# Kernel tuning notes

Measured on AMD Instinct MI355X. Metric: run time of the kernel, lower is better.

Reference implementation:

```python
import jax, jax.numpy as jnp
import numpy as np

N_NODES = 100000


def gcn_layer(x, edge_index, W, b):
    # GCNConv: out = D^{-1/2} (A + I) D^{-1/2} (x W) + b
    N = x.shape[0]
    loop = jnp.arange(N, dtype=edge_index.dtype)
    src = jnp.concatenate([edge_index[0], loop])
    dst = jnp.concatenate([edge_index[1], loop])
    deg = jax.ops.segment_sum(jnp.ones_like(src, dtype=x.dtype), dst, num_segments=N)
    dinv = jnp.where(deg > 0, jax.lax.rsqrt(deg), 0.0)
    norm = dinv[src] * dinv[dst]  # [E+N]
    h = x @ W  # [N, out]
    msg = h[src] * norm[:, None]  # [E+N, out]
    out = jax.ops.segment_sum(msg, dst, num_segments=N)
    return out + b


def setup_inputs() -> dict:
    key = jax.random.key(0)
    ks = jax.random.split(key, 8)
    x = jax.random.normal(ks[0], (N_NODES, 128), dtype=jnp.float32)
    edge_index = jax.random.randint(ks[1], (2, 1600000), 0, N_NODES, dtype=jnp.int32)
    def glorot(k, fan_in, fan_out):
        s = jnp.sqrt(6.0 / (fan_in + fan_out)).astype(jnp.float32)
        return jax.random.uniform(k, (fan_in, fan_out), jnp.float32, -s, s)
    return {
        "x": x,
        "edge_index": edge_index,
        "W1": glorot(ks[2], 128, 64), "b1": jnp.zeros((64,), jnp.float32),
        "W2": glorot(ks[3], 64, 128), "b2": jnp.zeros((128,), jnp.float32),
        "W3": glorot(ks[4], 128, 64), "b3": jnp.zeros((64,), jnp.float32),
    }


def reference(x, edge_index, W1, b1, W2, b2, W3, b3):
    h = jax.nn.relu(gcn_layer(x, edge_index, W1, b1))
    h = jax.nn.relu(gcn_layer(h, edge_index, W2, b2))
    out = gcn_layer(h, edge_index, W3, b3)
    return out
```

## Files before the change

kernel.cpp:

```cpp
#include <hip/hip_runtime.h>
#include <hip/hip_fp16.h>
#include <stdint.h>


#define NWGA 256
#define CMAX 8

typedef _Float16 half8 __attribute__((ext_vector_type(8)));
typedef float f32x4 __attribute__((ext_vector_type(4)));

struct __align__(8) Half4 { __half x, y, z, w; };

__global__ __launch_bounds__(256) void bucket_hist_kernel(
    const int* __restrict__ dst, int E, int chunk, int NBUK,
    int* __restrict__ M ) {
  __shared__ int hist[512];
  const int w = blockIdx.x, t = threadIdx.x;
  for (int i = t; i < NBUK; i += 256) hist[i] = 0;
  __syncthreads();
  const int e0 = w * chunk;
  const int e1 = min(e0 + chunk, E);
  for (int e = e0 + t; e < e1; e += 256) atomicAdd(&hist[dst[e] >> 8], 1);
  __syncthreads();
  for (int i = t; i < NBUK; i += 256) M[i * NWGA + w] = hist[i];
}

__global__ void scan_blocksum(const int* __restrict__ data, int len,
                              int* __restrict__ bsum) {
  __shared__ int s[256];
  int i = blockIdx.x * 256 + threadIdx.x;
  s[threadIdx.x] = (i < len) ? data[i] : 0;
  __syncthreads();
  for (int off = 128; off > 0; off >>= 1) {
    if (threadIdx.x < off) s[threadIdx.x] += s[threadIdx.x + off];
    __syncthreads();
  }
  if (threadIdx.x == 0) bsum[blockIdx.x] = s[0];
}

__global__ void scan_bsums(int* bsum, int NB) {
  __shared__ int s[512];
  int t = threadIdx.x;
  int v = (t < NB) ? bsum[t] : 0;
  s[t] = v;
  __syncthreads();
  for (int off = 1; off < 512; off <<= 1) {
    int u = (t >= off) ? s[t - off] : 0;
    __syncthreads();
    s[t] += u;
    __syncthreads();
  }
  if (t < NB) bsum[t] = s[t] - v;
}

__global__ void scan_final(int* __restrict__ data, int len,
                           const int* __restrict__ bsum) {
  __shared__ int s[256];
  int t = threadIdx.x;
  int i = blockIdx.x * 256 + t;
  int v = (i < len) ? data[i] : 0;
  s[t] = v;
  __syncthreads();
  for (int off = 1; off < 256; off <<= 1) {
    int u = (t >= off) ? s[t - off] : 0;
    __syncthreads();
    s[t] += u;
    __syncthreads();
  }
  if (i < len) data[i] = bsum[blockIdx.x] + s[t] - v;
}

__global__ __launch_bounds__(256) void bucket_scatter_kernel(
    const int* __restrict__ ei, int E, int chunk, int NBUK,
    const int* __restrict__ Mscan, int2* __restrict__ edata1) {
  __shared__ int cur[512];
  const int w = blockIdx.x, t = threadIdx.x;
  for (int i = t; i < NBUK; i += 256) cur[i] = Mscan[i * NWGA + w];
  __syncthreads();
  const int e0 = w * chunk;
  const int e1 = min(e0 + chunk, E);
  for (int e = e0 + t; e < e1; e += 256) {
    int s = ei[e];
    int d = ei[E + e];
    int pos = atomicAdd(&cur[d >> 8], 1);
    edata1[pos] = make_int2(s, d);
  }
}

__global__ __launch_bounds__(256) void bucket_deg_kernel(
    const int2* __restrict__ edata1, const int* __restrict__ Mscan, int E,
    int N, int NBUK, int* __restrict__ deg_arr, float* __restrict__ dinv,
    int* __restrict__ bsum2) {
  __shared__ int hist[256];
  __shared__ int red[256];
  const int b = blockIdx.x, t = threadIdx.x;
  const int ebase = Mscan[b * NWGA];
  const int eend = (b + 1 < NBUK) ? Mscan[(b + 1) * NWGA] : E;
  const int nodebase = b << 8;
  const int node = nodebase + t;
  hist[t] = 0;
  __syncthreads();
  for (int e = ebase + t; e < eend; e += 256)
    atomicAdd(&hist[edata1[e].y - nodebase], 1);
  __syncthreads();
  int pd = 0;
  if (node < N) {
    int dt = hist[t] + 1;
    pd = dt + (dt & 1);
    deg_arr[node] = dt;
    dinv[node] = rsqrtf((float)dt);
  }
  red[t] = pd;
  __syncthreads();
  for (int off = 128; off > 0; off >>= 1) {
    if (t < off) red[t] += red[t + off];
    __syncthreads();
  }
  if (t == 0) bsum2[b] = red[0];
}

__global__ void bucket_base_scan(int* bsum2, int NBUK, int* offsets, int N) {
  __shared__ int s[512];
  int t = threadIdx.x;
  int v = (t < NBUK) ? bsum2[t] : 0;
  s[t] = v;
  __syncthreads();
  for (int off = 1; off < 512; off <<= 1) {
    int u = (t >= off) ? s[t - off] : 0;
    __syncthreads();
    s[t] += u;
    __syncthreads();
  }
  if (t < NBUK) bsum2[t] = s[t] - v;
  if (t == NBUK - 1) offsets[N] = s[t];
}

__global__ __launch_bounds__(256) void bucket_fill_kernel(
    const int2* __restrict__ edata1, const int* __restrict__ Mscan,
    const int* __restrict__ deg_arr, const int* __restrict__ bsum2, int E,
    int N, int NBUK, int* __restrict__ offsets, int* __restrict__ ed3) {
  __shared__ int scan[256];
  __shared__ int cursor[256];
  const int b = blockIdx.x, t = threadIdx.x;
  const int ebase = Mscan[b * NWGA];
  const int eend = (b + 1 < NBUK) ? Mscan[(b + 1) * NWGA] : E;
  const int nodebase = b << 8;
  const int node = nodebase + t;
  const int dt = (node < N) ? deg_arr[node] : 0;
  const int pd = dt + (dt & 1);
  scan[t] = pd;
  __syncthreads();
  for (int off = 1; off < 256; off <<= 1) {
    int u = (t >= off) ? scan[t - off] : 0;
    __syncthreads();
    scan[t] += u;
    __syncthreads();
  }
  const int base = bsum2[b] + scan[t] - pd;
  cursor[t] = base + 1;
  if (node < N) {
    offsets[node] = base;
    ed3[base] = node << 7;
    if (dt & 1) ed3[base + dt] = N << 7;
  }
  __syncthreads();
  for (int e = ebase + t; e < eend; e += 256) {
    int2 sd = edata1[e];
    int pos = atomicAdd(&cursor[sd.y - nodebase], 1);
    ed3[pos] = sd.x << 7;
  }
}

__global__ void zero_rows_kernel(_Float16* a, _Float16* b) {
  if (threadIdx.x < 64) a[threadIdx.x] = (_Float16)0.f;
  else b[threadIdx.x - 64] = (_Float16)0.f;
}

template <int K, int D, bool BR, bool DSCALE, typename InT>
__global__ __launch_bounds__(256) void gemm_mfma(
    const InT* __restrict__ X, const float* __restrict__ W,
    const float* __restrict__ bias, const float* __restrict__ dinv,
    _Float16* __restrict__ H, int N) {
  __shared__ char lds[2 * K * D];
  const int t = threadIdx.x;
  for (int idx = t; idx < K * D; idx += 256) {
    const int k = idx % K;
    const int d = idx / K;
    const _Float16 v = (_Float16)W[k * D + d];
    const int byte =
        d * (2 * K) + ((((k >> 3) ^ (d & 7)) << 4) | ((k & 7) << 1));
    *(_Float16*)(lds + byte) = v;
  }
  __syncthreads();

  const int w = t >> 6;
  const int l = t & 63;
  const int lrow = l & 15;
  const int lg = l >> 4;
  const int r0 = blockIdx.x * 128 + w * 32;
  if (r0 >= N) return;

  f32x4 acc[2][D / 16];
#pragma unroll
  for (int rt = 0; rt < 2; ++rt)
#pragma unroll
    for (int c = 0; c < D / 16; ++c) acc[rt][c] = (f32x4){0.f, 0.f, 0.f, 0.f};

  int rA[2];
  rA[0] = min(r0 + lrow, N - 1);
  rA[1] = min(r0 + 16 + lrow, N - 1);

#pragma unroll
  for (int s = 0; s < K / 32; ++s) {
    half8 a[2];
#pragma unroll
    for (int rt = 0; rt < 2; ++rt) {
      if constexpr (sizeof(InT) == 2) {
        a[rt] = *reinterpret_cast<const half8*>(
            (const _Float16*)X + (size_t)rA[rt] * K + s * 32 + lg * 8);
      } else {
        const float* xp = (const float*)X + (size_t)rA[rt] * K + s * 32 + lg * 8;
        float4 lo = *reinterpret_cast<const float4*>(xp);
        float4 hi = *reinterpret_cast<const float4*>(xp + 4);
        half8 af;
        af[0] = (_Float16)lo.x; af[1] = (_Float16)lo.y;
        af[2] = (_Float16)lo.z; af[3] = (_Float16)lo.w;
        af[4] = (_Float16)hi.x; af[5] = (_Float16)hi.y;
        af[6] = (_Float16)hi.z; af[7] = (_Float16)hi.w;
        a[rt] = af;
      }
    }
    half8 b[D / 16];
#pragma unroll
    for (int c = 0; c < D / 16; ++c) {
      const int d = c * 16 + lrow;
      const int g = s * 4 + lg;
      b[c] = *reinterpret_cast<const half8*>(
          lds + d * (2 * K) + (((g ^ (d & 7)) << 4)));
    }
#pragma unroll
    for (int rt = 0; rt < 2; ++rt)
#pragma unroll
      for (int c = 0; c < D / 16; ++c)
        acc[rt][c] = __builtin_amdgcn_mfma_f32_16x16x32_f16(a[rt], b[c],
                                                            acc[rt][c], 0, 0, 0);
  }

  float bv[D / 16];
  if (BR) {
#pragma unroll
    for (int c = 0; c < D / 16; ++c) bv[c] = bias[c * 16 + lrow];
  }
#pragma unroll
  for (int rt = 0; rt < 2; ++rt) {
#pragma unroll
    for (int r = 0; r < 4; ++r) {
      const int row = r0 + rt * 16 + lg * 4 + r;
      if (row < N) {
        float ds = 1.f;
        if (DSCALE) ds = dinv[row];
#pragma unroll
        for (int c = 0; c < D / 16; ++c) {
          float v = acc[rt][c][r];
          if (BR) v = fmaxf(v + bv[c], 0.f);
          if (DSCALE) v *= ds;
          H[(size_t)row * D + c * 16 + lrow] = (_Float16)v;
        }
      }
    }
  }
}

template <bool BIAS, bool RELU, bool SCALE_OUT, typename OutT>
__global__ __launch_bounds__(256) void agg_kernel(
    const __half* __restrict__ h, const int* __restrict__ ed,
    const int* __restrict__ offsets, const float* __restrict__ dinv,
    const float* __restrict__ bias, OutT* __restrict__ out, int N) {
  const int wid = blockIdx.x * 4 + (threadIdx.x >> 6);
  const int na = wid * 8;
  if (na >= N) return;
  const int lane = threadIdx.x & 63;
  const int half32 = lane >> 5;
  const int fpair = lane & 31;
  const int nrem = min(8, N - na);

  const int off_l = offsets[na + min(lane, nrem)];
  const float dn_l = dinv[na + min(lane, nrem - 1)];
  const int eb0 = __shfl(off_l, 0);
  const int eb1 = __shfl(off_l, nrem);
  float2 bsv = make_float2(0.f, 0.f);
  if (BIAS) bsv = *reinterpret_cast<const float2*>(&bias[fpair * 2]);

  int pe[CMAX];
#pragma unroll
  for (int c = 0; c < CMAX; ++c) {
    int idx = eb0 + c * 64 + lane;
    pe[c] = ed[min(idx, eb1 - 1)];
  }

  const char* hb = (const char*)h + (fpair << 2);
  float ax = 0.f, ay = 0.f;
  int cur = 0;
  int bnd = __shfl(off_l, 1);
  float dn = __shfl(dn_l, 0);
  int j = eb0;

  auto flush = [&]() {
    float tx = ax + __shfl_xor(ax, 32);
    float ty = ay + __shfl_xor(ay, 32);
    float vx = tx * dn, vy = ty * dn;
    if (BIAS) { vx += bsv.x; vy += bsv.y; }
    if (RELU) { vx = fmaxf(vx, 0.f); vy = fmaxf(vy, 0.f); }
    if (SCALE_OUT) { vx *= dn; vy *= dn; }
    if (lane < 32) {
      if constexpr (sizeof(OutT) == 2) {
        *reinterpret_cast<__half2*>((char*)out + ((size_t)(na + cur) << 7) +
                                    (fpair << 2)) = __floats2half2_rn(vx, vy);
      } else {
        *reinterpret_cast<float2*>((char*)out + ((size_t)(na + cur) << 8) +
                                   (fpair << 3)) = make_float2(vx, vy);
      }
    }
    ax = 0.f; ay = 0.f;
    cur++;
    bnd = __shfl(off_l, min(cur + 1, 8));
    dn = __shfl(dn_l, min(cur, 7));
  };

#pragma unroll
  for (int c = 0; c < CMAX; ++c) {
    if (j < eb1) {
      const int pc = pe[c];
      for (int kp = 0; kp < 64; kp += 8) {
        if (j >= eb1) break;
        int so[4];
        float2 g[4];
#pragma unroll
        for (int i = 0; i < 4; ++i)
          so[i] = __shfl(pc, kp + 2 * i + half32);
#pragma unroll
        for (int i = 0; i < 4; ++i)
          g[i] = __half22float2(*reinterpret_cast<const __half2*>(
              hb + (size_t)(unsigned)so[i]));
#pragma unroll
        for (int i = 0; i < 4; ++i) {
          if (j + 2 * i == bnd) flush();
          ax += g[i].x;
          ay += g[i].y;
        }
        j += 8;
      }
    }
  }
  for (; j < eb1; j += 2) {
    int so = ed[j + half32];
    float2 g = __half22float2(
        *reinterpret_cast<const __half2*>(hb + (size_t)(unsigned)so));
    if (j == bnd) flush();
    ax += g.x;
    ay += g.y;
  }
  if (cur < nrem) flush();
}

extern "C" void kernel_launch(void* const* d_in, const int* in_sizes, int n_in,
                              void* d_out, int out_size, void* d_ws,
                              size_t ws_size, hipStream_t stream) {
  const float* x  = (const float*)d_in[0];
  const int*   ei = (const int*)d_in[1];
  const float* W1 = (const float*)d_in[2];
  const float* b1 = (const float*)d_in[3];
  const float* W2 = (const float*)d_in[4];
  const float* b2 = (const float*)d_in[5];
  const float* W3 = (const float*)d_in[6];
  const float* b3 = (const float*)d_in[7];

  const int N = in_sizes[0] / 128;
  const int E = in_sizes[1] / 2;
  const int NBUK = (N + 255) >> 8;
  const int MLEN = NBUK * NWGA;
  const int chunk = (E + NWGA - 1) / NWGA;

  char* w = (char*)d_ws;
  int* offsets = (int*)w;      w += (size_t)(N + 2) * 4;
  float* dinv = (float*)w;     w += (size_t)N * 4;
  int* deg_arr = (int*)w;      w += (size_t)N * 4;
  int* bsum2 = (int*)w;        w += 512 * 4;
  w = (char*)(((uintptr_t)w + 255) & ~(uintptr_t)255);
  int* edata3 = (int*)w;       w += (size_t)(E + 2 * N) * 4;
  w = (char*)(((uintptr_t)w + 255) & ~(uintptr_t)255);
  char* regionA = w;           w += (size_t)(N + 1) * 64 * 2;
  w = (char*)(((uintptr_t)w + 255) & ~(uintptr_t)255);
  char* regionB = w;           w += (size_t)E * 8;
  w = (char*)(((uintptr_t)w + 255) & ~(uintptr_t)255);
  char* regionC = w;           w += (size_t)N * 128 * 2;

  int* M = (int*)regionA;
  int* bsum = M + MLEN;
  _Float16* ht1 = (_Float16*)regionA;
  int2* edata1 = (int2*)regionB;
  _Float16* a2 = (_Float16*)regionB;
  _Float16* hout1 = (_Float16*)regionC;
  _Float16* h2 = (_Float16*)regionC;

  const int NBS = (MLEN + 255) / 256;
  const int NW = (N + 7) / 8;
  const int AGB = (NW + 3) / 4;
  const int GGB = (N + 127) / 128;

  zero_rows_kernel<<<1, 128, 0, stream>>>(ht1 + (size_t)N * 64,
                                          hout1 + (size_t)N * 64);
  bucket_hist_kernel<<<NWGA, 256, 0, stream>>>(ei + E, E, chunk, NBUK, M);
  scan_blocksum<<<NBS, 256, 0, stream>>>(M, MLEN, bsum);
  scan_bsums<<<1, 512, 0, stream>>>(bsum, NBS);
  scan_final<<<NBS, 256, 0, stream>>>(M, MLEN, bsum);
  bucket_scatter_kernel<<<NWGA, 256, 0, stream>>>(ei, E, chunk, NBUK, M, edata1);
  bucket_deg_kernel<<<NBUK, 256, 0, stream>>>(edata1, M, E, N, NBUK, deg_arr,
                                              dinv, bsum2);
  bucket_base_scan<<<1, 512, 0, stream>>>(bsum2, NBUK, offsets, N);
  bucket_fill_kernel<<<NBUK, 256, 0, stream>>>(edata1, M, deg_arr, bsum2, E, N,
                                               NBUK, offsets, edata3);

  gemm_mfma<128, 64, false, true, float><<<GGB, 256, 0, stream>>>(
      x, W1, nullptr, dinv, ht1, N);
  agg_kernel<true, true, true, __half><<<AGB, 256, 0, stream>>>(
      (const __half*)ht1, edata3, offsets, dinv, b1, (__half*)hout1, N);

  agg_kernel<false, false, false, __half><<<AGB, 256, 0, stream>>>(
      (const __half*)hout1, edata3, offsets, dinv, nullptr, (__half*)a2, N);
  gemm_mfma<64, 128, true, false, _Float16><<<GGB, 256, 0, stream>>>(
      a2, W2, b2, nullptr, h2, N);

  gemm_mfma<128, 64, false, true, _Float16><<<GGB, 256, 0, stream>>>(
      h2, W3, nullptr, dinv, ht1, N);
  agg_kernel<true, false, false, float><<<AGB, 256, 0, stream>>>(
      (const __half*)ht1, edata3, offsets, dinv, b3, (float*)d_out, N);
}
```

Baseline: 323.4 us.

## Gather 8-byte fp16 quads per lane in aggregation with 4-edge padded CSR

The aggregation kernel now has each lane gather four fp16 features (8 bytes) per edge, so four edges are processed per wavefront step instead of two. To keep edge boundaries aligned with that stride, each node's CSR segment is padded to a multiple of four with entries pointing at a zero row. The partial sums are then reduced across four lane groups with two xor shuffles per component. This trades more padding entries and extra shuffles for fewer, wider memory transactions and half as many loop iterations over the edges.

```diff
diff --git a/kernel.cpp b/kernel.cpp
--- a/kernel.cpp
+++ b/kernel.cpp
@@ -106,7 +106,7 @@
   int pd = 0;
   if (node < N) {
     int dt = hist[t] + 1;
-    pd = dt + (dt & 1);
+    pd = (dt + 3) & ~3;
     deg_arr[node] = dt;
     dinv[node] = rsqrtf((float)dt);
   }
@@ -147,7 +147,7 @@
   const int nodebase = b << 8;
   const int node = nodebase + t;
   const int dt = (node < N) ? deg_arr[node] : 0;
-  const int pd = dt + (dt & 1);
+  const int pd = (dt + 3) & ~3;
   scan[t] = pd;
   __syncthreads();
   for (int off = 1; off < 256; off <<= 1) {
@@ -161,7 +161,7 @@
   if (node < N) {
     offsets[node] = base;
     ed3[base] = node << 7;
-    if (dt & 1) ed3[base + dt] = N << 7;
+    for (int p = dt; p < pd; ++p) ed3[base + p] = N << 7;
   }
   __syncthreads();
   for (int e = ebase + t; e < eend; e += 256) {
@@ -280,16 +280,16 @@
   const int na = wid * 8;
   if (na >= N) return;
   const int lane = threadIdx.x & 63;
-  const int half32 = lane >> 5;
-  const int fpair = lane & 31;
+  const int grp = lane >> 4;
+  const int fq = lane & 15;
   const int nrem = min(8, N - na);
 
   const int off_l = offsets[na + min(lane, nrem)];
   const float dn_l = dinv[na + min(lane, nrem - 1)];
   const int eb0 = __shfl(off_l, 0);
   const int eb1 = __shfl(off_l, nrem);
-  float2 bsv = make_float2(0.f, 0.f);
-  if (BIAS) bsv = *reinterpret_cast<const float2*>(&bias[fpair * 2]);
+  float4 bsv = make_float4(0.f, 0.f, 0.f, 0.f);
+  if (BIAS) bsv = *reinterpret_cast<const float4*>(&bias[fq * 4]);
 
   int pe[CMAX];
 #pragma unroll
@@ -298,30 +298,39 @@
     pe[c] = ed[min(idx, eb1 - 1)];
   }
 
-  const char* hb = (const char*)h + (fpair << 2);
-  float ax = 0.f, ay = 0.f;
+  const char* hb = (const char*)h + (fq << 3);
+  float4 acc = make_float4(0.f, 0.f, 0.f, 0.f);
   int cur = 0;
   int bnd = __shfl(off_l, 1);
   float dn = __shfl(dn_l, 0);
   int j = eb0;
 
   auto flush = [&]() {
-    float tx = ax + __shfl_xor(ax, 32);
-    float ty = ay + __shfl_xor(ay, 32);
-    float vx = tx * dn, vy = ty * dn;
-    if (BIAS) { vx += bsv.x; vy += bsv.y; }
-    if (RELU) { vx = fmaxf(vx, 0.f); vy = fmaxf(vy, 0.f); }
-    if (SCALE_OUT) { vx *= dn; vy *= dn; }
-    if (lane < 32) {
+    float sx = acc.x, sy = acc.y, sz = acc.z, sw = acc.w;
+    sx += __shfl_xor(sx, 16); sx += __shfl_xor(sx, 32);
+    sy += __shfl_xor(sy, 16); sy += __shfl_xor(sy, 32);
+    sz += __shfl_xor(sz, 16); sz += __shfl_xor(sz, 32);
+    sw += __shfl_xor(sw, 16); sw += __shfl_xor(sw, 32);
+    float vx = sx * dn, vy = sy * dn, vz = sz * dn, vw = sw * dn;
+    if (BIAS) { vx += bsv.x; vy += bsv.y; vz += bsv.z; vw += bsv.w; }
+    if (RELU) {
+      vx = fmaxf(vx, 0.f); vy = fmaxf(vy, 0.f);
+      vz = fmaxf(vz, 0.f); vw = fmaxf(vw, 0.f);
+    }
+    if (SCALE_OUT) { vx *= dn; vy *= dn; vz *= dn; vw *= dn; }
+    if (lane < 16) {
       if constexpr (sizeof(OutT) == 2) {
-        *reinterpret_cast<__half2*>((char*)out + ((size_t)(na + cur) << 7) +
-                                    (fpair << 2)) = __floats2half2_rn(vx, vy);
+        __half2 h0 = __floats2half2_rn(vx, vy);
+        __half2 h1 = __floats2half2_rn(vz, vw);
+        uint2 pk = make_uint2(*(unsigned int*)&h0, *(unsigned int*)&h1);
+        *reinterpret_cast<uint2*>((char*)out + ((size_t)(na + cur) << 7) +
+                                  (fq << 3)) = pk;
       } else {
-        *reinterpret_cast<float2*>((char*)out + ((size_t)(na + cur) << 8) +
-                                   (fpair << 3)) = make_float2(vx, vy);
+        *reinterpret_cast<float4*>((char*)out + ((size_t)(na + cur) << 8) +
+                                   (fq << 4)) = make_float4(vx, vy, vz, vw);
       }
     }
-    ax = 0.f; ay = 0.f;
+    acc = make_float4(0.f, 0.f, 0.f, 0.f);
     cur++;
     bnd = __shfl(off_l, min(cur + 1, 8));
     dn = __shfl(dn_l, min(cur, 7));
@@ -331,34 +340,33 @@
   for (int c = 0; c < CMAX; ++c) {
     if (j < eb1) {
       const int pc = pe[c];
-      for (int kp = 0; kp < 64; kp += 8) {
+      for (int kb = 0; kb < 64; kb += 16) {
         if (j >= eb1) break;
         int so[4];
-        float2 g[4];
-#pragma unroll
-        for (int i = 0; i < 4; ++i)
-          so[i] = __shfl(pc, kp + 2 * i + half32);
-#pragma unroll
-        for (int i = 0; i < 4; ++i)
-          g[i] = __half22float2(*reinterpret_cast<const __half2*>(
-              hb + (size_t)(unsigned)so[i]));
-#pragma unroll
-        for (int i = 0; i < 4; ++i) {
-          if (j + 2 * i == bnd) flush();
-          ax += g[i].x;
-          ay += g[i].y;
+        uint2 gq[4];
+#pragma unroll
+        for (int q = 0; q < 4; ++q) so[q] = __shfl(pc, kb + 4 * q + grp);
+#pragma unroll
+        for (int q = 0; q < 4; ++q)
+          gq[q] = *reinterpret_cast<const uint2*>(hb + (size_t)(unsigned)so[q]);
+#pragma unroll
+        for (int q = 0; q < 4; ++q) {
+          if (j == bnd) flush();
+          float2 lo = __half22float2(*reinterpret_cast<__half2*>(&gq[q].x));
+          float2 hi = __half22float2(*reinterpret_cast<__half2*>(&gq[q].y));
+          acc.x += lo.x; acc.y += lo.y; acc.z += hi.x; acc.w += hi.y;
+          j += 4;
         }
-        j += 8;
       }
     }
   }
-  for (; j < eb1; j += 2) {
-    int so = ed[j + half32];
-    float2 g = __half22float2(
-        *reinterpret_cast<const __half2*>(hb + (size_t)(unsigned)so));
+  for (; j < eb1; j += 4) {
+    int so = ed[j + grp];
+    uint2 g = *reinterpret_cast<const uint2*>(hb + (size_t)(unsigned)so);
     if (j == bnd) flush();
-    ax += g.x;
-    ay += g.y;
+    float2 lo = __half22float2(*reinterpret_cast<__half2*>(&g.x));
+    float2 hi = __half22float2(*reinterpret_cast<__half2*>(&g.y));
+    acc.x += lo.x; acc.y += lo.y; acc.z += hi.x; acc.w += hi.y;
   }
   if (cur < nrem) flush();
 }
@@ -387,7 +395,7 @@
   int* deg_arr = (int*)w;      w += (size_t)N * 4;
   int* bsum2 = (int*)w;        w += 512 * 4;
   w = (char*)(((uintptr_t)w + 255) & ~(uintptr_t)255);
-  int* edata3 = (int*)w;       w += (size_t)(E + 2 * N) * 4;
+  int* edata3 = (int*)w;       w += (size_t)(E + 4 * N + 64) * 4;
   w = (char*)(((uintptr_t)w + 255) & ~(uintptr_t)255);
   char* regionA = w;           w += (size_t)(N + 1) * 64 * 2;
   w = (char*)(((uintptr_t)w + 255) & ~(uintptr_t)255);
```

New measurement: 319.7 us. No clear change (-1.1%).
